# Optimization experiments

Hardware: AMD Instinct MI355X
Metric: run time of the kernel (lower is better)

## Reference

```python
import jax, jax.numpy as jnp
import numpy as np

NUM_HEADS = 12


def get_rel_pos(q_size, k_size, rel_pos):
    # rel_pos: (2*max(q,k)-1, C). Here q_size==k_size so no interpolation needed.
    q_coords = jnp.arange(q_size)[:, None] * max(k_size / q_size, 1.0)
    k_coords = jnp.arange(k_size)[None, :] * max(q_size / k_size, 1.0)
    rel = (q_coords - k_coords) + (k_size - 1) * max(q_size / k_size, 1.0)
    return rel_pos[rel.astype(jnp.int32)]  # (q_size, k_size, C)


def add_decomposed_rel_pos(attn, q, rel_pos_h, rel_pos_w, q_size, k_size):
    q_h, q_w = q_size
    k_h, k_w = k_size
    Rh = get_rel_pos(q_h, k_h, rel_pos_h)  # (q_h,k_h,C)
    Rw = get_rel_pos(q_w, k_w, rel_pos_w)  # (q_w,k_w,C)
    B, _, C = q.shape  # B = num_heads * batch
    r_q = q.reshape(B, q_h, q_w, C)
    rel_h = jnp.einsum('bhwc,hkc->bhwk', r_q, Rh)  # (B,q_h,q_w,k_h)
    rel_w = jnp.einsum('bhwc,wkc->bhwk', r_q, Rw)  # (B,q_h,q_w,k_w)
    attn = attn.reshape(B, q_h, q_w, k_h, k_w)
    attn = attn + rel_h[:, :, :, :, None] + rel_w[:, :, :, None, :]
    return attn.reshape(B, q_h * q_w, k_h * k_w)


def setup_inputs() -> dict:
    key = jax.random.key(0)
    ks = jax.random.split(key, 7)
    B, H, W, dim = 128, 14, 14, 768
    head_dim = dim // NUM_HEADS
    return {
        'x': jax.random.normal(ks[0], (B, H, W, dim), dtype=jnp.float32),
        'qkv_w': jax.random.normal(ks[1], (dim, 3 * dim), dtype=jnp.float32) * 0.02,
        'qkv_b': jax.random.normal(ks[2], (3 * dim,), dtype=jnp.float32) * 0.02,
        'proj_w': jax.random.normal(ks[3], (dim, dim), dtype=jnp.float32) * 0.02,
        'proj_b': jax.random.normal(ks[4], (dim,), dtype=jnp.float32) * 0.02,
        'rel_pos_h': jax.random.normal(ks[5], (2 * H - 1, head_dim), dtype=jnp.float32) * 0.02,
        'rel_pos_w': jax.random.normal(ks[6], (2 * W - 1, head_dim), dtype=jnp.float32) * 0.02,
    }


def reference(x, qkv_w, qkv_b, proj_w, proj_b, rel_pos_h, rel_pos_w):
    B, H, W, dim = x.shape
    nh = NUM_HEADS
    hd = dim // nh
    scale = hd ** -0.5
    L = H * W
    # qkv projection: (B,H,W,3*dim) -> (3, nh*B, L, hd)
    qkv = x.reshape(B, L, dim) @ qkv_w + qkv_b
    qkv = qkv.reshape(B, L, 3, nh, hd)
    qkv = jnp.transpose(qkv, (2, 3, 0, 1, 4)).reshape(3, nh * B, L, hd)
    q, k, v = qkv[0], qkv[1], qkv[2]
    attn = jnp.einsum('bqc,bkc->bqk', q * scale, k)  # (nh*B, L, L)
    attn = add_decomposed_rel_pos(attn, q, rel_pos_h, rel_pos_w, (H, W), (H, W))
    attn = jax.nn.softmax(attn, axis=-1)
    out = jnp.einsum('bqk,bkc->bqc', attn, v)  # (nh*B, L, hd)
    out = out.reshape(nh, B, H, W, hd)
    out = jnp.transpose(out, (1, 2, 3, 0, 4)).reshape(B, H, W, dim)
    return out @ proj_w + proj_b
```

## Files before the change

### kernel.cpp

```cpp
#include <hip/hip_runtime.h>
#include <stdint.h>
#include <math.h>

typedef unsigned short u16;
typedef __bf16 bf16x8 __attribute__((ext_vector_type(8)));
typedef u16 u16x8 __attribute__((ext_vector_type(8)));
typedef float f32x4 __attribute__((ext_vector_type(4)));

#define MFMA16(a,b,c) __builtin_amdgcn_mfma_f32_16x16x32_bf16((a),(b),(c),0,0,0)
#define GLOAD16(gp, lp) __builtin_amdgcn_global_load_lds( \
    (const __attribute__((address_space(1))) void*)(gp), \
    (__attribute__((address_space(3))) void*)(lp), 16, 0, 0)
#define BARRIER_FENCED() asm volatile("s_barrier" ::: "memory")

__device__ __forceinline__ u16 f2bf(float f) {
  union { float f; uint32_t u; } v; v.f = f;
  return (u16)((v.u + 0x7FFFu + ((v.u >> 16) & 1u)) >> 16);
}
__device__ __forceinline__ float bits2f(uint32_t u) {
  union { uint32_t u; float f; } v; v.u = u; return v.f;
}
__device__ __forceinline__ uint32_t cvtpk(float lo, float hi) {
  uint32_t r;
  asm("v_cvt_pk_bf16_f32 %0, %1, %2" : "=v"(r) : "v"(lo), "v"(hi));
  return r;
}
__device__ __forceinline__ int4 pack8(const u16* v) {
  int4 r;
  r.x = (int)((uint32_t)v[0] | ((uint32_t)v[1] << 16));
  r.y = (int)((uint32_t)v[2] | ((uint32_t)v[3] << 16));
  r.z = (int)((uint32_t)v[4] | ((uint32_t)v[5] << 16));
  r.w = (int)((uint32_t)v[6] | ((uint32_t)v[7] << 16));
  return r;
}

__global__ void k_cvt(const float* __restrict__ in, u16* __restrict__ out, int n4, float scale) {
  int i = blockIdx.x * 256 + threadIdx.x;
  int stride = gridDim.x * 256;
  for (; i < n4; i += stride) {
    float4 v = reinterpret_cast<const float4*>(in)[i];
    ushort4 o;
    o.x = f2bf(v.x * scale); o.y = f2bf(v.y * scale);
    o.z = f2bf(v.z * scale); o.w = f2bf(v.w * scale);
    reinterpret_cast<ushort4*>(out)[i] = o;
  }
}

__global__ void k_transpose(const float* __restrict__ in, u16* __restrict__ out, int R, int C) {
  __shared__ float t[32][33];
  int tx = threadIdx.x & 31, ty = threadIdx.x >> 5;
  int c0 = blockIdx.x * 32, r0 = blockIdx.y * 32;
  #pragma unroll
  for (int i = 0; i < 4; i++)
    t[ty + i*8][tx] = in[(size_t)(r0 + ty + i*8) * C + (c0 + tx)];
  __syncthreads();
  #pragma unroll
  for (int i = 0; i < 4; i++)
    out[(size_t)(c0 + ty + i*8) * R + (r0 + tx)] = f2bf(t[tx][ty + i*8]);
}

__global__ __launch_bounds__(512, 2) void k_qkv256(
    const u16* __restrict__ A, const u16* __restrict__ BT, const float* __restrict__ bias,
    u16* __restrict__ qo, u16* __restrict__ ko, u16* __restrict__ vo)
{
  __shared__ u16 SMEM[65536];

  int bid0 = blockIdx.x;
  int xcd = bid0 & 7, idx = bid0 >> 3;
  int base = (xcd < 2) ? xcd * 111 : 2 * 111 + (xcd - 2) * 110;
  int wgid = base + idx;
  int mt = wgid / 9, nt = wgid - (wgid / 9) * 9;

  int tid = threadIdx.x, lane = tid & 63, w = tid >> 6;
  int g = lane >> 4, c4 = lane & 15;
  int wr = w >> 2, wc = w & 3;

  int strow = tid >> 3;
  int sslot = (tid & 7) ^ ((tid >> 3) & 7);
  const u16* pA[4];
  const u16* pB[4];
  #pragma unroll
  for (int c = 0; c < 4; c++) {
    pA[c] = A + (size_t)(mt * 256 + c * 64 + strow) * 768 + sslot * 8;
    pB[c] = BT + (size_t)(nt * 256 + c * 64 + strow) * 768 + sslot * 8;
  }
  int ldsw = w * 512;

  int rs0 = (g ^ (c4 & 7)) * 8;
  int rs1 = ((4 + g) ^ (c4 & 7)) * 8;
  int abase = wr * 8192 + c4 * 64;
  int bbase = 32768 + (wc >> 1) * 8192 + ((wc & 1) * 64 + c4) * 64;

  f32x4 acc[8][4];
  f32x4 z4 = {0.f, 0.f, 0.f, 0.f};
  #pragma unroll
  for (int f = 0; f < 8; f++)
    #pragma unroll
    for (int fc = 0; fc < 4; fc++) acc[f][fc] = z4;

#define STAGE_QKV(KT)                                                        \
  {                                                                          \
    u16* ab_ = SMEM + ((KT) & 1) * 16384 + ldsw;                             \
    u16* bb_ = SMEM + 32768 + ((KT) & 1) * 16384 + ldsw;                     \
    _Pragma("unroll") for (int c_ = 0; c_ < 4; c_++)                         \
      GLOAD16(pA[c_] + (KT) * 64, ab_ + c_ * 4096);                          \
    _Pragma("unroll") for (int c_ = 0; c_ < 4; c_++)                         \
      GLOAD16(pB[c_] + (KT) * 64, bb_ + c_ * 4096);                          \
  }

  STAGE_QKV(0)
  STAGE_QKV(1)
  asm volatile("s_waitcnt vmcnt(8)" ::: "memory");
  BARRIER_FENCED();

  for (int kt = 0; kt < 12; ++kt) {
    const u16* Td = SMEM + (kt & 1) * 16384;
    bf16x8 a0[8], b0[4], a1[8], b1[4];
    #pragma unroll
    for (int f = 0; f < 8; f++) a0[f] = *(const bf16x8*)(Td + abase + f * 1024 + rs0);
    #pragma unroll
    for (int n = 0; n < 4; n++) b0[n] = *(const bf16x8*)(Td + bbase + n * 1024 + rs0);
    __builtin_amdgcn_sched_barrier(0);
    #pragma unroll
    for (int f = 0; f < 8; f++) a1[f] = *(const bf16x8*)(Td + abase + f * 1024 + rs1);
    #pragma unroll
    for (int n = 0; n < 4; n++) b1[n] = *(const bf16x8*)(Td + bbase + n * 1024 + rs1);

    asm volatile("s_waitcnt lgkmcnt(12)" ::: "memory");
    __builtin_amdgcn_sched_barrier(0);
    __builtin_amdgcn_s_setprio(1);
    #pragma unroll
    for (int f = 0; f < 8; f++)
      #pragma unroll
      for (int fc = 0; fc < 4; fc++)
        acc[f][fc] = MFMA16(a0[f], b0[fc], acc[f][fc]);
    __builtin_amdgcn_s_setprio(0);

    asm volatile("s_waitcnt lgkmcnt(0)" ::: "memory");
    __builtin_amdgcn_sched_barrier(0);
    BARRIER_FENCED();

    if (kt < 10) STAGE_QKV(kt + 2)

    __builtin_amdgcn_s_setprio(1);
    #pragma unroll
    for (int f = 0; f < 8; f++)
      #pragma unroll
      for (int fc = 0; fc < 4; fc++)
        acc[f][fc] = MFMA16(a1[f], b1[fc], acc[f][fc]);
    __builtin_amdgcn_s_setprio(0);

    if (kt < 10)       { asm volatile("s_waitcnt vmcnt(8)" ::: "memory"); }
    else if (kt == 10) { asm volatile("s_waitcnt vmcnt(0)" ::: "memory"); }
    __builtin_amdgcn_sched_barrier(0);
    BARRIER_FENCED();
  }
#undef STAGE_QKV

  int i3 = nt / 3;
  u16* dst = (i3 == 0) ? qo : (i3 == 1) ? ko : vo;
  int head = (nt - i3 * 3) * 4 + wc;
  float bsv[4];
  #pragma unroll
  for (int fc = 0; fc < 4; fc++) bsv[fc] = bias[nt * 256 + wc * 64 + fc * 16 + c4];

  int mbase = mt * 256 + wr * 128 + g * 4;
  #pragma unroll
  for (int f = 0; f < 8; f++) {
    #pragma unroll
    for (int j = 0; j < 4; j++) {
      int mm = mbase + f * 16 + j;
      int bb2 = mm / 196, ll = mm - bb2 * 196;
      size_t ro = (size_t)((head * 128 + bb2) * 196 + ll) * 64;
      #pragma unroll
      for (int fc = 0; fc < 4; fc++)
        dst[ro + fc * 16 + c4] = f2bf(acc[f][fc][j] + bsv[fc]);
    }
  }
}

__device__ __forceinline__ void rd_frags8(const u16* As_, const u16* Bs_, int aoff, int boff,
                                          bf16x8 (&b)[4], bf16x8 (&a)[4]) {
  #pragma unroll
  for (int fc = 0; fc < 4; fc++) b[fc] = *(const bf16x8*)(Bs_ + boff + fc * 512);
  #pragma unroll
  for (int f = 0; f < 4; f++) a[f] = *(const bf16x8*)(As_ + aoff + f * 512);
}

__global__ __launch_bounds__(256, 2) void k_proj256(
    const u16* __restrict__ A, const u16* __restrict__ BT, const float* __restrict__ bias,
    float* __restrict__ out)
{
  __shared__ u16 SMEM[32768];

  int bid0 = blockIdx.x;
  int bid = (bid0 & 7) * 147 + (bid0 >> 3);
  int nt = bid % 6, mt = bid / 6;

  int tid = threadIdx.x, lane = tid & 63, w = tid >> 6;
  int g = lane >> 4, c4 = lane & 15;
  int wr = w >> 1, wc = w & 1;

  int srow = lane >> 2;
  int pslot = (lane & 3) ^ ((lane >> 3) & 3);
  int cidA = w * 2;

  const u16* pA1 = A + (size_t)(mt * 128 + cidA * 16 + srow) * 768 + pslot * 8;
  const u16* pA2 = pA1 + 16 * 768;
  const u16* pB1 = BT + (size_t)(nt * 128 + cidA * 16 + srow) * 768 + pslot * 8;
  const u16* pB2 = pB1 + 16 * 768;

  int rsel = g ^ ((c4 >> 1) & 3);
  int aoff = wr * 2048 + c4 * 32 + rsel * 8;
  int boff = wc * 2048 + c4 * 32 + rsel * 8;

  f32x4 acc[4][4];
  f32x4 z4 = {0.f, 0.f, 0.f, 0.f};
  #pragma unroll
  for (int f = 0; f < 4; f++)
    #pragma unroll
    for (int fc = 0; fc < 4; fc++) acc[f][fc] = z4;

  #pragma unroll
  for (int kk = 0; kk < 3; kk++) {
    u16* dA = SMEM + kk * 4096;
    GLOAD16(pA1 + kk * 32, dA + cidA * 512);
    GLOAD16(pA2 + kk * 32, dA + (cidA + 1) * 512);
    u16* dB = SMEM + 16384 + kk * 4096;
    GLOAD16(pB1 + kk * 32, dB + cidA * 512);
    GLOAD16(pB2 + kk * 32, dB + (cidA + 1) * 512);
  }
  asm volatile("s_waitcnt vmcnt(8)" ::: "memory");
  __builtin_amdgcn_s_barrier();

  for (int k = 0; k < 24; ++k) {
    const u16* As = SMEM + (k & 3) * 4096;
    const u16* Bs = SMEM + 16384 + (k & 3) * 4096;
    bf16x8 bfr[4], afr[4];
    rd_frags8(As, Bs, aoff, boff, bfr, afr);
    if (k < 21) {
      u16* dA = SMEM + ((k + 3) & 3) * 4096;
      GLOAD16(pA1 + (k + 3) * 32, dA + cidA * 512);
      GLOAD16(pA2 + (k + 3) * 32, dA + (cidA + 1) * 512);
      u16* dB = SMEM + 16384 + ((k + 3) & 3) * 4096;
      GLOAD16(pB1 + (k + 3) * 32, dB + cidA * 512);
      GLOAD16(pB2 + (k + 3) * 32, dB + (cidA + 1) * 512);
      asm volatile("s_waitcnt vmcnt(8)" ::: "memory");
    } else if (k == 21) {
      asm volatile("s_waitcnt vmcnt(4)" ::: "memory");
    } else if (k == 22) {
      asm volatile("s_waitcnt vmcnt(0)" ::: "memory");
    }
    __builtin_amdgcn_s_barrier();
    __builtin_amdgcn_s_setprio(1);
    #pragma unroll
    for (int f = 0; f < 4; f++)
      #pragma unroll
      for (int fc = 0; fc < 4; fc++)
        acc[f][fc] = MFMA16(afr[f], bfr[fc], acc[f][fc]);
    __builtin_amdgcn_s_setprio(0);
    __builtin_amdgcn_s_barrier();
  }

  #pragma unroll
  for (int fc = 0; fc < 4; fc++) {
    int n0 = nt * 128 + wc * 64 + fc * 16 + c4;
    float bs = bias[n0];
    #pragma unroll
    for (int fr = 0; fr < 4; fr++)
      #pragma unroll
      for (int j = 0; j < 4; j++) {
        int m = mt * 128 + wr * 64 + fr * 16 + g * 4 + j;
        out[(size_t)m * 768 + n0] = acc[fr][fc][j] + bs;
      }
  }
}

#define VP 232
__global__ __launch_bounds__(256, 2) void k_attn(
    const u16* __restrict__ Q, const u16* __restrict__ Kg, const u16* __restrict__ Vg,
    const u16* __restrict__ RPH, const u16* __restrict__ RPW, u16* __restrict__ Ows)
{
  __shared__ u16 K64[208 * 64];
  __shared__ u16 Krel[208 * 40];
  __shared__ u16 VT[64 * VP];
  __shared__ u16 Qrel[4][16 * 40];

  int bh = blockIdx.x;
  int hh = bh >> 7, bb = bh & 127;
  int tid = threadIdx.x, lane = tid & 63, w = tid >> 6;
  int g = lane >> 4, c4 = lane & 15;

  const u16* kbase = Kg + (size_t)bh * 12544;
  const u16* vbase = Vg + (size_t)bh * 12544;
  const u16* qbase = Q + (size_t)bh * 12544;

  const float KSC = 0.18033688011f;
  for (int ch = tid; ch < 1664; ch += 256) {
    int row = ch >> 3, s = ch & 7;
    u16 outv[8];
    if (row < 196) {
      u16x8 v = *(const u16x8*)(kbase + row * 64 + s * 8);
      #pragma unroll
      for (int e = 0; e < 8; e++)
        outv[e] = f2bf(bits2f((uint32_t)v[e] << 16) * KSC);
    } else {
      #pragma unroll
      for (int e = 0; e < 8; e++) outv[e] = 0;
    }
    *(int4*)(K64 + row * 64 + ((s ^ (row & 7)) * 8)) = pack8(outv);
  }
  if (tid < 208) {
    int k = tid;
    int kh = k / 14, kw2 = k - kh * 14;
    #pragma unroll
    for (int s = 0; s < 5; s++) {
      u16 vals[8];
      #pragma unroll
      for (int e = 0; e < 8; e++) {
        int c = s * 8 + e;
        u16 x = 0;
        if (k < 196) {
          if (c == kh) x = 0x3F80;
          else if (c == 14 + kw2) x = 0x3F80;
        } else {
          if (c == 28) x = 0x3F80;
        }
        vals[e] = x;
      }
      *(int4*)(Krel + k * 40 + s * 8) = pack8(vals);
    }
  }
  for (int i = tid; i < 2048; i += 256) {
    int chn = i >> 5, c = 192 + (i & 31);
    if (c >= 196 && c < VP) VT[chn * VP + c] = 0;
  }
  for (int ch2 = tid; ch2 < 784; ch2 += 256) {
    int kp = ch2 % 98, cb = ch2 / 98;
    int key = kp * 2, cz = cb * 8;
    u16x8 a = *(const u16x8*)(vbase + key * 64 + cz);
    u16x8 b2 = *(const u16x8*)(vbase + (key + 1) * 64 + cz);
    int kk = key & 31;
    int colp = (key >> 5) * 32 + ((kk & 15) >> 2) * 8 + (kk & 3) + ((kk >> 4) << 2);
    #pragma unroll
    for (int j = 0; j < 8; j++) {
      uint32_t pk = (uint32_t)a[j] | ((uint32_t)b2[j] << 16);
      *(uint32_t*)(VT + (cz + j) * VP + colp) = pk;
    }
  }
  __syncthreads();

  int t1 = 16 + c4; if (t1 > 26) t1 = 26;
  bf16x8 rh00 = *(const bf16x8*)(RPH + c4 * 64 + g * 8);
  bf16x8 rh01 = *(const bf16x8*)(RPH + c4 * 64 + 32 + g * 8);
  bf16x8 rh10 = *(const bf16x8*)(RPH + t1 * 64 + g * 8);
  bf16x8 rh11 = *(const bf16x8*)(RPH + t1 * 64 + 32 + g * 8);
  bf16x8 rw00 = *(const bf16x8*)(RPW + c4 * 64 + g * 8);
  bf16x8 rw01 = *(const bf16x8*)(RPW + c4 * 64 + 32 + g * 8);
  bf16x8 rw10 = *(const bf16x8*)(RPW + t1 * 64 + g * 8);
  bf16x8 rw11 = *(const bf16x8*)(RPW + t1 * 64 + 32 + g * 8);

  f32x4 z4 = {0.f, 0.f, 0.f, 0.f};

  int qi0 = w * 16 + c4;
  int qr0 = qi0 > 195 ? 195 : qi0;
  bf16x8 qa0 = *(const bf16x8*)(qbase + qr0 * 64 + g * 8);
  bf16x8 qa1 = *(const bf16x8*)(qbase + qr0 * 64 + 32 + g * 8);

  for (int qt = w; qt < 13; qt += 4) {
    int qi = qt * 16 + c4;
    bf16x8 nq0, nq1;
    int qn = qt + 4;
    if (qn < 13) {
      int qrn = qn * 16 + c4; if (qrn > 195) qrn = 195;
      nq0 = *(const bf16x8*)(qbase + qrn * 64 + g * 8);
      nq1 = *(const bf16x8*)(qbase + qrn * 64 + 32 + g * 8);
    }

    u16* Qr = (u16*)Qrel[w];
    {
      int4 zz = {0, 0, 0, 0};
      *(int4*)(Qr + lane * 8) = zz;
      if (lane < 16) *(int4*)(Qr + 512 + lane * 8) = zz;
      if (g == 0) Qr[c4 * 40 + 28] = f2bf(-30000.f);
    }

    int qh = qi / 14;
    int qwv = qi - qh * 14;

    f32x4 e0 = MFMA16(rh00, qa0, z4); e0 = MFMA16(rh01, qa1, e0);
    f32x4 e1 = MFMA16(rh10, qa0, z4); e1 = MFMA16(rh11, qa1, e1);
    #pragma unroll
    for (int tt = 0; tt < 2; tt++) {
      f32x4 e = tt ? e1 : e0;
      #pragma unroll
      for (int j = 0; j < 4; j++) {
        int t = tt * 16 + 4 * g + j;
        int kh = qh + 13 - t;
        if ((unsigned)kh <= 13u) Qr[c4 * 40 + kh] = f2bf(e[j]);
      }
    }
    f32x4 f0 = MFMA16(rw00, qa0, z4); f0 = MFMA16(rw01, qa1, f0);
    f32x4 f1 = MFMA16(rw10, qa0, z4); f1 = MFMA16(rw11, qa1, f1);
    #pragma unroll
    for (int tt = 0; tt < 2; tt++) {
      f32x4 e = tt ? f1 : f0;
      #pragma unroll
      for (int j = 0; j < 4; j++) {
        int t = tt * 16 + 4 * g + j;
        int kw3 = qwv + 13 - t;
        if ((unsigned)kw3 <= 13u) Qr[c4 * 40 + 14 + kw3] = f2bf(e[j]);
      }
    }

    bf16x8 qrelB = *(const bf16x8*)(Qr + c4 * 40 + g * 8);

    f32x4 St[13];
    #pragma unroll
    for (int i = 0; i < 13; i++) {
      int key = i * 16 + c4;
      const u16* kr = K64 + key * 64;
      int sw = key & 7;
      bf16x8 kb0 = *(const bf16x8*)(kr + ((g ^ sw) * 8));
      bf16x8 kb1 = *(const bf16x8*)(kr + (((4 + g) ^ sw) * 8));
      f32x4 acc = MFMA16(kb0, qa0, z4);
      acc = MFMA16(kb1, qa1, acc);
      bf16x8 krl = *(const bf16x8*)(Krel + key * 40 + g * 8);
      St[i] = MFMA16(krl, qrelB, acc);
    }

    float mx = -3.0e38f;
    #pragma unroll
    for (int i = 0; i < 13; i++)
      #pragma unroll
      for (int j = 0; j < 4; j++) mx = fmaxf(mx, St[i][j]);
    mx = fmaxf(mx, __shfl_xor(mx, 16));
    mx = fmaxf(mx, __shfl_xor(mx, 32));

    float ls = 0.f;
    f32x4 O[4] = {z4, z4, z4, z4};
    #pragma unroll
    for (int p = 0; p < 7; p++) {
      float pe[8];
      #pragma unroll
      for (int j2 = 0; j2 < 4; j2++) { pe[j2] = exp2f(St[2 * p][j2] - mx); ls += pe[j2]; }
      if (p < 6) {
        #pragma unroll
        for (int j2 = 0; j2 < 4; j2++) { pe[4 + j2] = exp2f(St[2 * p + 1][j2] - mx); ls += pe[4 + j2]; }
      } else {
        #pragma unroll
        for (int j2 = 0; j2 < 4; j2++) pe[4 + j2] = 0.f;
      }
      union { uint32_t u[4]; bf16x8 v; } pb;
      pb.u[0] = cvtpk(pe[0], pe[1]);
      pb.u[1] = cvtpk(pe[2], pe[3]);
      pb.u[2] = cvtpk(pe[4], pe[5]);
      pb.u[3] = cvtpk(pe[6], pe[7]);
      #pragma unroll
      for (int ct = 0; ct < 4; ct++) {
        bf16x8 va = *(const bf16x8*)(VT + (ct * 16 + c4) * VP + p * 32 + g * 8);
        O[ct] = MFMA16(va, pb.v, O[ct]);
      }
    }
    ls += __shfl_xor(ls, 16);
    ls += __shfl_xor(ls, 32);

    if (qi < 196) {
      float inv = 1.f / ls;
      size_t obase = (size_t)(bb * 196 + qi) * 768 + hh * 64;
      #pragma unroll
      for (int ct = 0; ct < 4; ct++) {
        uint32_t o0 = cvtpk(O[ct][0] * inv, O[ct][1] * inv);
        uint32_t o1 = cvtpk(O[ct][2] * inv, O[ct][3] * inv);
        uint2 ov = {o0, o1};
        *(uint2*)(Ows + obase + ct * 16 + g * 4) = ov;
      }
    }
    qa0 = nq0; qa1 = nq1;
  }
}

extern "C" void kernel_launch(void* const* d_in, const int* in_sizes, int n_in,
                              void* d_out, int out_size, void* d_ws, size_t ws_size,
                              hipStream_t stream) {
  (void)in_sizes; (void)n_in; (void)out_size; (void)ws_size;
  const float* x      = (const float*)d_in[0];
  const float* qkv_w  = (const float*)d_in[1];
  const float* qkv_b  = (const float*)d_in[2];
  const float* proj_w = (const float*)d_in[3];
  const float* proj_b = (const float*)d_in[4];
  const float* rph    = (const float*)d_in[5];
  const float* rpw    = (const float*)d_in[6];
  float* out = (float*)d_out;
  char* ws = (char*)d_ws;

  u16* xb   = (u16*)(ws);
  u16* wT   = (u16*)(ws + 38535168);
  u16* pT   = (u16*)(ws + 42074112);
  u16* rphb = (u16*)(ws + 43253760);
  u16* rpwb = (u16*)(ws + 43257856);
  u16* qws  = (u16*)(ws + 43261952);
  u16* kws  = (u16*)(ws + 81797120);
  u16* vws  = (u16*)(ws + 120332288);
  u16* Ows  = xb;

  const float LOG2E = 1.44269504f;
  k_cvt<<<2048, 256, 0, stream>>>(x, xb, 4816896, 1.0f);
  k_cvt<<<2, 256, 0, stream>>>(rph, rphb, 432, LOG2E);
  k_cvt<<<2, 256, 0, stream>>>(rpw, rpwb, 432, LOG2E);
  k_transpose<<<dim3(72, 24), 256, 0, stream>>>(qkv_w, wT, 768, 2304);
  k_transpose<<<dim3(24, 24), 256, 0, stream>>>(proj_w, pT, 768, 768);
  k_qkv256<<<882, 512, 0, stream>>>(xb, wT, qkv_b, qws, kws, vws);
  k_attn<<<1536, 256, 0, stream>>>(qws, kws, vws, rphb, rpwb, Ows);
  k_proj256<<<1176, 256, 0, stream>>>(Ows, pT, proj_b, out);
}
```

Baseline: 273.0 us.

## Split QKV GEMM k-tile into quarter phases with staggered half-tile prefetch

Restructures the QKV projection main loop into four sub-phases per k-tile. Each phase loads a quarter of the A/B fragments from LDS and issues one half-tile global-to-LDS prefetch, with finer-grained waitcnt and barriers in between. The aim is to interleave LDS reads, global loads and MFMAs more evenly and to reduce register pressure from holding full fragment sets. It adds more barriers per k-tile and has more intricate buffer-reuse timing, which risks stalls or races if the wait counts are wrong.

Result: no change. 270.0 us (-1.1%).

```diff
diff --git a/kernel.cpp b/kernel.cpp
--- a/kernel.cpp
+++ b/kernel.cpp
@@ -12,6 +12,9 @@
     (const __attribute__((address_space(1))) void*)(gp), \
     (__attribute__((address_space(3))) void*)(lp), 16, 0, 0)
 #define BARRIER_FENCED() asm volatile("s_barrier" ::: "memory")
+#define SB0() __builtin_amdgcn_sched_barrier(0)
+#define LGK(N) do { asm volatile("s_waitcnt lgkmcnt(" #N ")" ::: "memory"); SB0(); } while(0)
+#define VW(N)  do { asm volatile("s_waitcnt vmcnt(" #N ")"  ::: "memory"); SB0(); } while(0)
 
 __device__ __forceinline__ u16 f2bf(float f) {
   union { float f; uint32_t u; } v; v.f = f;
@@ -67,7 +70,7 @@
 
   int bid0 = blockIdx.x;
   int xcd = bid0 & 7, idx = bid0 >> 3;
-  int base = (xcd < 2) ? xcd * 111 : 2 * 111 + (xcd - 2) * 110;
+  int base = (xcd < 2) ? xcd * 111 : 222 + (xcd - 2) * 110;
   int wgid = base + idx;
   int mt = wgid / 9, nt = wgid - (wgid / 9) * 9;
 
@@ -75,21 +78,17 @@
   int g = lane >> 4, c4 = lane & 15;
   int wr = w >> 2, wc = w & 3;
 
-  int strow = tid >> 3;
-  int sslot = (tid & 7) ^ ((tid >> 3) & 7);
-  const u16* pA[4];
-  const u16* pB[4];
-  #pragma unroll
-  for (int c = 0; c < 4; c++) {
-    pA[c] = A + (size_t)(mt * 256 + c * 64 + strow) * 768 + sslot * 8;
-    pB[c] = BT + (size_t)(nt * 256 + c * 64 + strow) * 768 + sslot * 8;
-  }
+  int st = tid >> 3;
+  int sg = (tid & 7) ^ ((tid >> 3) & 7);
+  const u16* pAs = A  + (size_t)(mt * 256 + st) * 768 + sg * 8;
+  const u16* pBs = BT + (size_t)(nt * 256 + st) * 768 + sg * 8;
   int ldsw = w * 512;
 
   int rs0 = (g ^ (c4 & 7)) * 8;
   int rs1 = ((4 + g) ^ (c4 & 7)) * 8;
-  int abase = wr * 8192 + c4 * 64;
-  int bbase = 32768 + (wc >> 1) * 8192 + ((wc & 1) * 64 + c4) * 64;
+  int c464 = c4 * 64;
+  int aHalf = wr * 8192;
+  int bHalf = 32768 + (wc >> 1) * 8192 + (wc & 1) * 4096;
 
   f32x4 acc[8][4];
   f32x4 z4 = {0.f, 0.f, 0.f, 0.f};
@@ -98,64 +97,120 @@
     #pragma unroll
     for (int fc = 0; fc < 4; fc++) acc[f][fc] = z4;
 
-#define STAGE_QKV(KT)                                                        \
-  {                                                                          \
-    u16* ab_ = SMEM + ((KT) & 1) * 16384 + ldsw;                             \
-    u16* bb_ = SMEM + 32768 + ((KT) & 1) * 16384 + ldsw;                     \
-    _Pragma("unroll") for (int c_ = 0; c_ < 4; c_++)                         \
-      GLOAD16(pA[c_] + (KT) * 64, ab_ + c_ * 4096);                          \
-    _Pragma("unroll") for (int c_ = 0; c_ < 4; c_++)                         \
-      GLOAD16(pB[c_] + (KT) * 64, bb_ + c_ * 4096);                          \
-  }
-
-  STAGE_QKV(0)
-  STAGE_QKV(1)
-  asm volatile("s_waitcnt vmcnt(8)" ::: "memory");
+#define STG(T, ISB, H)                                                        \
+  {                                                                           \
+    const u16* s_ = ((ISB) ? pBs : pAs) + (size_t)((H) * 128) * 768 + (T) * 64; \
+    u16* d_ = SMEM + ((ISB) ? 32768 : 0) + ((T) & 1) * 16384 + (H) * 8192 + ldsw; \
+    GLOAD16(s_, d_);                                                          \
+    GLOAD16(s_ + (size_t)64 * 768, d_ + 4096);                                \
+  }
+
+  STG(0, 0, 0) STG(0, 0, 1) STG(0, 1, 0) STG(0, 1, 1) STG(1, 1, 0) STG(1, 0, 0)
+  VW(0);
   BARRIER_FENCED();
 
-  for (int kt = 0; kt < 12; ++kt) {
-    const u16* Td = SMEM + (kt & 1) * 16384;
-    bf16x8 a0[8], b0[4], a1[8], b1[4];
-    #pragma unroll
-    for (int f = 0; f < 8; f++) a0[f] = *(const bf16x8*)(Td + abase + f * 1024 + rs0);
-    #pragma unroll
-    for (int n = 0; n < 4; n++) b0[n] = *(const bf16x8*)(Td + bbase + n * 1024 + rs0);
-    __builtin_amdgcn_sched_barrier(0);
-    #pragma unroll
-    for (int f = 0; f < 8; f++) a1[f] = *(const bf16x8*)(Td + abase + f * 1024 + rs1);
-    #pragma unroll
-    for (int n = 0; n < 4; n++) b1[n] = *(const bf16x8*)(Td + bbase + n * 1024 + rs1);
-
-    asm volatile("s_waitcnt lgkmcnt(12)" ::: "memory");
-    __builtin_amdgcn_sched_barrier(0);
-    __builtin_amdgcn_s_setprio(1);
-    #pragma unroll
-    for (int f = 0; f < 8; f++)
-      #pragma unroll
-      for (int fc = 0; fc < 4; fc++)
-        acc[f][fc] = MFMA16(a0[f], b0[fc], acc[f][fc]);
-    __builtin_amdgcn_s_setprio(0);
-
-    asm volatile("s_waitcnt lgkmcnt(0)" ::: "memory");
-    __builtin_amdgcn_sched_barrier(0);
-    BARRIER_FENCED();
-
-    if (kt < 10) STAGE_QKV(kt + 2)
-
-    __builtin_amdgcn_s_setprio(1);
-    #pragma unroll
-    for (int f = 0; f < 8; f++)
-      #pragma unroll
-      for (int fc = 0; fc < 4; fc++)
-        acc[f][fc] = MFMA16(a1[f], b1[fc], acc[f][fc]);
-    __builtin_amdgcn_s_setprio(0);
-
-    if (kt < 10)       { asm volatile("s_waitcnt vmcnt(8)" ::: "memory"); }
-    else if (kt == 10) { asm volatile("s_waitcnt vmcnt(0)" ::: "memory"); }
-    __builtin_amdgcn_sched_barrier(0);
-    BARRIER_FENCED();
-  }
-#undef STAGE_QKV
+#define TILE(KT, S12, S34, VM3, VM4)                                          \
+  {                                                                           \
+    const u16* Ad = SMEM + ((KT) & 1) * 16384 + aHalf;                        \
+    const u16* Bd = SMEM + ((KT) & 1) * 16384 + bHalf;                        \
+    bf16x8 a0[4], a1[4], bb[8];                                               \
+                  \
+    _Pragma("unroll") for (int mf = 0; mf < 4; mf++)                          \
+      a0[mf] = *(const bf16x8*)(Ad + mf * 1024 + c464 + rs0);                 \
+    bb[0] = *(const bf16x8*)(Bd + c464 + rs0);                                \
+    bb[2] = *(const bf16x8*)(Bd + 1024 + c464 + rs0);                         \
+    SB0();                                                                    \
+    _Pragma("unroll") for (int mf = 0; mf < 4; mf++)                          \
+      a1[mf] = *(const bf16x8*)(Ad + mf * 1024 + c464 + rs1);                 \
+    bb[1] = *(const bf16x8*)(Bd + c464 + rs1);                                \
+    bb[3] = *(const bf16x8*)(Bd + 1024 + c464 + rs1);                         \
+    SB0();                                                                    \
+    if (S12) STG((KT) + 1, 1, 1)                                              \
+    LGK(6);                                                                   \
+    __builtin_amdgcn_s_setprio(1);                                            \
+    _Pragma("unroll") for (int mf = 0; mf < 4; mf++) {                        \
+      acc[mf][0] = MFMA16(a0[mf], bb[0], acc[mf][0]);                         \
+      acc[mf][1] = MFMA16(a0[mf], bb[2], acc[mf][1]);                         \
+    }                                                                         \
+    __builtin_amdgcn_s_setprio(0);                                            \
+    LGK(0);                                                                   \
+    __builtin_amdgcn_s_setprio(1);                                            \
+    _Pragma("unroll") for (int mf = 0; mf < 4; mf++) {                        \
+      acc[mf][0] = MFMA16(a1[mf], bb[1], acc[mf][0]);                         \
+      acc[mf][1] = MFMA16(a1[mf], bb[3], acc[mf][1]);                         \
+    }                                                                         \
+    __builtin_amdgcn_s_setprio(0);                                            \
+    VW(4);                                                                    \
+    BARRIER_FENCED();                                                         \
+                  \
+    bb[4] = *(const bf16x8*)(Bd + 2048 + c464 + rs0);                         \
+    bb[6] = *(const bf16x8*)(Bd + 3072 + c464 + rs0);                         \
+    SB0();                                                                    \
+    bb[5] = *(const bf16x8*)(Bd + 2048 + c464 + rs1);                         \
+    bb[7] = *(const bf16x8*)(Bd + 3072 + c464 + rs1);                         \
+    SB0();                                                                    \
+    if (S12) STG((KT) + 1, 0, 1)                                              \
+    LGK(2);                                                                   \
+    __builtin_amdgcn_s_setprio(1);                                            \
+    _Pragma("unroll") for (int mf = 0; mf < 4; mf++) {                        \
+      acc[mf][2] = MFMA16(a0[mf], bb[4], acc[mf][2]);                         \
+      acc[mf][3] = MFMA16(a0[mf], bb[6], acc[mf][3]);                         \
+    }                                                                         \
+    __builtin_amdgcn_s_setprio(0);                                            \
+    LGK(0);                                                                   \
+    __builtin_amdgcn_s_setprio(1);                                            \
+    _Pragma("unroll") for (int mf = 0; mf < 4; mf++) {                        \
+      acc[mf][2] = MFMA16(a1[mf], bb[5], acc[mf][2]);                         \
+      acc[mf][3] = MFMA16(a1[mf], bb[7], acc[mf][3]);                         \
+    }                                                                         \
+    __builtin_amdgcn_s_setprio(0);                                            \
+    VW(4);                                                                    \
+    BARRIER_FENCED();                                                         \
+                  \
+    _Pragma("unroll") for (int mf = 0; mf < 4; mf++)                          \
+      a0[mf] = *(const bf16x8*)(Ad + (4 + mf) * 1024 + c464 + rs0);           \
+    SB0();                                                                    \
+    _Pragma("unroll") for (int mf = 0; mf < 4; mf++)                          \
+      a1[mf] = *(const bf16x8*)(Ad + (4 + mf) * 1024 + c464 + rs1);           \
+    SB0();                                                                    \
+    if (S34) STG((KT) + 2, 1, 0)                                              \
+    LGK(4);                                                                   \
+    __builtin_amdgcn_s_setprio(1);                                            \
+    _Pragma("unroll") for (int mf = 0; mf < 4; mf++) {                        \
+      acc[4 + mf][0] = MFMA16(a0[mf], bb[0], acc[4 + mf][0]);                 \
+      acc[4 + mf][1] = MFMA16(a0[mf], bb[2], acc[4 + mf][1]);                 \
+    }                                                                         \
+    __builtin_amdgcn_s_setprio(0);                                            \
+    LGK(0);                                                                   \
+    __builtin_amdgcn_s_setprio(1);                                            \
+    _Pragma("unroll") for (int mf = 0; mf < 4; mf++) {                        \
+      acc[4 + mf][0] = MFMA16(a1[mf], bb[1], acc[4 + mf][0]);                 \
+      acc[4 + mf][1] = MFMA16(a1[mf], bb[3], acc[4 + mf][1]);                 \
+    }                                                                         \
+    __builtin_amdgcn_s_setprio(0);                                            \
+    VM3;                                                                      \
+    BARRIER_FENCED();                                                         \
+        \
+    if (S34) STG((KT) + 2, 0, 0)                                              \
+    __builtin_amdgcn_s_setprio(1);                                            \
+    _Pragma("unroll") for (int mf = 0; mf < 4; mf++) {                        \
+      acc[4 + mf][2] = MFMA16(a0[mf], bb[4], acc[4 + mf][2]);                 \
+      acc[4 + mf][3] = MFMA16(a0[mf], bb[6], acc[4 + mf][3]);                 \
+      acc[4 + mf][2] = MFMA16(a1[mf], bb[5], acc[4 + mf][2]);                 \
+      acc[4 + mf][3] = MFMA16(a1[mf], bb[7], acc[4 + mf][3]);                 \
+    }                                                                         \
+    __builtin_amdgcn_s_setprio(0);                                            \
+    VM4;                                                                      \
+    BARRIER_FENCED();                                                         \
+  }
+
+  for (int kt = 0; kt < 10; ++kt) {
+    TILE(kt, 1, 1, VW(4), VW(4))
+  }
+  TILE(10, 1, 0, VW(2), VW(0))
+  TILE(11, 0, 0, (void)0, (void)0)
+#undef TILE
+#undef STG
 
   int i3 = nt / 3;
   u16* dst = (i3 == 0) ? qo : (i3 == 1) ? ko : vo;
```
